# Kernel tuning notes

Measured on AMD Instinct MI355X. Metric: run time of the kernel, lower is better.

The kernel has to match this reference:

```python
import jax, jax.numpy as jnp
import numpy as np

B, NPG, DEG = 512, 128, 16          # graphs, nodes/graph, out-degree
N = B * NPG                          # 65536 nodes
E = N * DEG                          # 1048576 edges
IN_DIM, HID, HEADS = 11, 32, 4
K1 = int(np.ceil(0.8 * NPG))         # 103 nodes/graph after pool1
K2 = int(np.ceil(0.8 * K1))          # 83 nodes/graph after pool2


def gat_conv(x, src, dst, mask, W, a_s, a_d, b, n_nodes):
    # PyG GATConv (concat=True, add_self_loops=True, eval mode -> no dropout)
    xp = (x @ W).reshape(n_nodes, HEADS, HID)            # [N,H,C]
    as_ = jnp.einsum('nhc,hc->nh', xp, a_s)
    ad_ = jnp.einsum('nhc,hc->nh', xp, a_d)
    loop = jnp.arange(n_nodes)
    s = jnp.concatenate([src, loop])
    d = jnp.concatenate([dst, loop])
    m = jnp.concatenate([mask, jnp.ones(n_nodes, bool)])
    logit = jax.nn.leaky_relu(as_[s] + ad_[d], 0.2)      # [E+N,H]
    logit = jnp.where(m[:, None], logit, -1e9)
    mx = jax.ops.segment_max(logit, d, num_segments=n_nodes)
    ex = jnp.exp(logit - mx[d]) * m[:, None]
    den = jax.ops.segment_sum(ex, d, num_segments=n_nodes)
    alpha = ex / (den[d] + 1e-16)                        # segment softmax over dst
    out = jax.ops.segment_sum(alpha[:, :, None] * xp[s], d, num_segments=n_nodes)
    return out.reshape(n_nodes, HEADS * HID) + b


def topk_pool(x, src, dst, mask, w, npg, k):
    # PyG TopKPooling: score = tanh((x*w).sum(-1)/||w||); keep top ceil(ratio*n) per graph
    nb = x.shape[0] // npg
    score = jnp.tanh((x @ w) / jnp.linalg.norm(w))
    vals, idx = jax.lax.top_k(score.reshape(nb, npg), k)  # [B,k]
    perm = (idx + (jnp.arange(nb) * npg)[:, None]).reshape(-1)
    x_new = x[perm] * vals.reshape(-1, 1)
    remap = jnp.full(nb * npg, -1).at[perm].set(jnp.arange(nb * k))
    ns, nd = remap[src], remap[dst]
    m = mask & (ns >= 0) & (nd >= 0)
    return x_new, jnp.where(m, ns, 0), jnp.where(m, nd, 0), m


def setup_inputs():
    key = jax.random.key(0)
    ks = jax.random.split(key, 24)
    s = 0.05
    x = jax.random.normal(ks[0], (N, IN_DIM), jnp.float32)
    src = jnp.repeat(jnp.arange(N), DEG)
    dst = (src // NPG) * NPG + jax.random.randint(ks[1], (E,), 0, NPG)
    edge_index = jnp.stack([src, dst])
    edge_attr = jax.random.normal(ks[2], (E, 4), jnp.float32)
    batch = jnp.repeat(jnp.arange(B), NPG)
    p = dict(
        W_g1=jax.random.normal(ks[3], (IN_DIM, HEADS * HID), jnp.float32) * s,
        att_src1=jax.random.normal(ks[4], (HEADS, HID), jnp.float32) * s,
        att_dst1=jax.random.normal(ks[5], (HEADS, HID), jnp.float32) * s,
        b_g1=jnp.zeros((HEADS * HID,), jnp.float32),
        W_t1=jax.random.normal(ks[6], (HEADS * HID, HID), jnp.float32) * s,
        b_t1=jnp.zeros((HID,), jnp.float32),
        pool_w1=jax.random.normal(ks[7], (HID,), jnp.float32) * s,
        W_g2=jax.random.normal(ks[8], (HID, HEADS * HID), jnp.float32) * s,
        att_src2=jax.random.normal(ks[9], (HEADS, HID), jnp.float32) * s,
        att_dst2=jax.random.normal(ks[10], (HEADS, HID), jnp.float32) * s,
        b_g2=jnp.zeros((HEADS * HID,), jnp.float32),
        W_t2=jax.random.normal(ks[11], (HEADS * HID, HID), jnp.float32) * s,
        b_t2=jnp.zeros((HID,), jnp.float32),
        pool_w2=jax.random.normal(ks[12], (HID,), jnp.float32) * s,
        W_l1=jax.random.normal(ks[13], (2 * HID, 256), jnp.float32) * s,
        b_l1=jnp.zeros((256,), jnp.float32),
        W_l2=jax.random.normal(ks[14], (256, 1024), jnp.float32) * s,
        b_l2=jnp.zeros((1024,), jnp.float32),
        W_l3=jax.random.normal(ks[15], (1024, 1), jnp.float32) * s,
        b_l3=jnp.zeros((1,), jnp.float32),
    )
    return dict(x=x, edge_index=edge_index, edge_attr=edge_attr, batch=batch, **p)


def reference(x, edge_index, edge_attr, batch,
              W_g1, att_src1, att_dst1, b_g1, W_t1, b_t1, pool_w1,
              W_g2, att_src2, att_dst2, b_g2, W_t2, b_t2, pool_w2,
              W_l1, b_l1, W_l2, b_l2, W_l3, b_l3):
    # edge_attr is ignored (GATConv built without edge_dim); batch is implicit
    # in the fixed equal-size graph layout.  Eval mode -> dropout disabled.
    src, dst = edge_index[0], edge_index[1]
    mask = jnp.ones(E, bool)
    h = jax.nn.relu(gat_conv(x, src, dst, mask, W_g1, att_src1, att_dst1, b_g1, N))
    h = h @ W_t1 + b_t1
    h, src, dst, mask = topk_pool(h, src, dst, mask, pool_w1, NPG, K1)
    h1 = h.reshape(B, K1, HID)
    g1 = jnp.concatenate([h1.max(1), h1.mean(1)], axis=1)   # [B, 2*HID]
    h = jax.nn.relu(gat_conv(h, src, dst, mask, W_g2, att_src2, att_dst2, b_g2, B * K1))
    h = h @ W_t2 + b_t2
    h, src, dst, mask = topk_pool(h, src, dst, mask, pool_w2, K1, K2)
    h2 = h.reshape(B, K2, HID)
    g2 = jnp.concatenate([h2.max(1), h2.mean(1)], axis=1)
    g = g1 + g2
    g = jax.nn.relu(g @ W_l1 + b_l1)
    g = jax.nn.relu(g @ W_l2 + b_l2)
    return g @ W_l3 + b_l3                                   # [B,1]
```

## Files before the change

kernel.cpp:

```cpp
#include <hip/hip_runtime.h>
#include <math.h>

constexpr int NPGc  = 128;
constexpr int NG    = 512;
constexpr int EPGc  = 2048;
constexpr int ETOT  = 1048576;
constexpr int IND   = 11;
constexpr int HIDc  = 32;
constexpr int FD    = 128;
constexpr int K1c   = 103;
constexpr int K2c   = 83;
constexpr int NN    = NG * NPGc;
constexpr int N2c   = NG * K1c;
constexpr int EPAD  = 2432;
constexpr int SBCAP = 2560;
constexpr int OFFSTR= 264;

__device__ __forceinline__ float lrelu(float x){ return fmaxf(x, 0.2f*x); }

template<int KIN>
__device__ void foldDev(const float* __restrict__ Wg, const float* __restrict__ avs,
                        const float* __restrict__ avd, float* __restrict__ S, float* __restrict__ D, int t)
{
    if (t < KIN * 4) {
        int k = t >> 2, h = t & 3;
        float s = 0.f, d = 0.f;
        for (int j = 0; j < HIDc; j++) {
            float w = Wg[k*FD + h*HIDc + j];
            s = fmaf(w, avs[h*HIDc + j], s);
            d = fmaf(w, avd[h*HIDc + j], d);
        }
        S[t] = s; D[t] = d;
    }
}

__global__ __launch_bounds__(256) void k_prep(const int* __restrict__ ei,
    const float* __restrict__ W1g, const float* __restrict__ s1, const float* __restrict__ d1,
    const float* __restrict__ W2g, const float* __restrict__ s2, const float* __restrict__ d2,
    int* __restrict__ csrOff, unsigned char* __restrict__ csrSB,
    float* __restrict__ S1, float* __restrict__ D1, float* __restrict__ S2, float* __restrict__ D2)
{
    int b = blockIdx.x, t = threadIdx.x;
    if (b >= NG) {
        if (b == NG)     foldDev<IND>(W1g, s1, d1, S1, D1, t);
        else             foldDev<HIDc>(W2g, s2, d2, S2, D2, t);
        return;
    }
    int g = b;
    __shared__ int cnt[128], cur[128], offL[129];
    __shared__ __align__(16) unsigned char sbL[SBCAP];
    const int FILL1 = (int)0x80808080u;
    if (t < 128) cnt[t] = 0;
    if (t < SBCAP/16) ((int4*)sbL)[t] = make_int4(FILL1, FILL1, FILL1, FILL1);
    __syncthreads();
    const int* dstG = ei + ETOT + g * EPGc;
    int dnv[8];
    #pragma unroll
    for (int q = 0; q < 8; q++) {
        int e = t + 256*q;
        dnv[q] = dstG[e] - g * NPGc;
        atomicAdd(&cnt[dnv[q]], 1);
    }
    __syncthreads();
    if (t < 64) {
        int c0 = cnt[2*t], c1 = cnt[2*t + 1];
        int p0 = (c0 + 3) & ~3, p1 = (c1 + 3) & ~3;
        int ps = p0 + p1, P = ps;
        #pragma unroll
        for (int dl = 1; dl < 64; dl <<= 1) { int v = __shfl_up(P, dl); if (t >= dl) P += v; }
        int E0 = P - ps;
        offL[2*t] = E0; offL[2*t + 1] = E0 + p0;
        cur[2*t]  = E0; cur[2*t + 1]  = E0 + p0;
        if (t == 63) offL[128] = P;
    }
    __syncthreads();
    #pragma unroll
    for (int q = 0; q < 8; q++) {
        int e = t + 256*q;
        int pos = atomicAdd(&cur[dnv[q]], 1);
        sbL[pos] = (unsigned char)(e >> 4);
    }
    __syncthreads();
    if (t < SBCAP/16) ((int4*)(csrSB + (size_t)g * SBCAP))[t] = ((const int4*)sbL)[t];
    if (t <= 128) csrOff[g*OFFSTR + t] = offL[t];
    if (t < 128)  csrOff[g*OFFSTR + 132 + t] = cur[t];
}

template<int NNODE, int KIN>
__global__ __launch_bounds__(256) void k_gat(
    const float* __restrict__ xin, const float* __restrict__ Wg,
    const float* __restrict__ WsS, const float* __restrict__ WsD,
    const int* __restrict__ csrOff, const unsigned char* __restrict__ csrSB,
    const float* __restrict__ bias, const float* __restrict__ Wt,
    float* __restrict__ htp)
{
    int g = blockIdx.x, h = blockIdx.y, t = threadIdx.x;
    __shared__ __align__(16) float xpL[NNODE * 32];
    __shared__ __align__(16) float WL[KIN * 32];
    __shared__ __align__(16) unsigned char sbL[SBCAP];
    __shared__ float asL[NNODE + 1], adL[NNODE], mL[NNODE], dIL[NNODE];
    __shared__ unsigned short offL[NNODE + 1];

    const float* xg = xin + (size_t)g * NNODE * KIN;

    for (int i = t; i < KIN * 32; i += 256) { int k = i >> 5, c = i & 31; WL[i] = Wg[k*FD + h*32 + c]; }
    if (t <= NNODE) offL[t] = (unsigned short)csrOff[g*OFFSTR + t];
    if (t < SBCAP/16) ((int4*)sbL)[t] = ((const int4*)(csrSB + (size_t)g * SBCAP))[t];
    if (t == NNODE) asL[NNODE] = -1e30f;
    __syncthreads();

    for (int p = t; p < NNODE * 8; p += 256) {
        int n = p >> 3, c4 = p & 7;
        const float* xr = xg + (size_t)n * KIN;
        float4 acc = make_float4(0.f, 0.f, 0.f, 0.f);
        #pragma unroll
        for (int k = 0; k < KIN; k++) {
            float xv = xr[k];
            float4 w4 = *(const float4*)&WL[k*32 + c4*4];
            acc.x = fmaf(xv, w4.x, acc.x); acc.y = fmaf(xv, w4.y, acc.y);
            acc.z = fmaf(xv, w4.z, acc.z); acc.w = fmaf(xv, w4.w, acc.w);
        }
        ((float4*)xpL)[n*8 + (c4 ^ (n & 7))] = acc;
    }
    if (t < NNODE) {
        const float* xr = xg + (size_t)t * KIN;
        float s = 0.f, d = 0.f;
        #pragma unroll
        for (int k = 0; k < KIN; k++) { float v = xr[k]; s = fmaf(v, WsS[k*4 + h], s); d = fmaf(v, WsD[k*4 + h], d); }
        asL[t] = s; adL[t] = d;
    }
    __syncthreads();

    if (t < NNODE) {
        float as_n = asL[t], adn = adL[t];
        int lo = offL[t], hi = offL[t + 1];
        float mx = as_n;
        for (int i = lo; i < hi; i += 4) {
            unsigned int q4 = *(const unsigned int*)(sbL + i);
            float a0 = asL[q4 & 255], a1 = asL[(q4 >> 8) & 255];
            float a2 = asL[(q4 >> 16) & 255], a3 = asL[q4 >> 24];
            mx = fmaxf(fmaxf(fmaxf(fmaxf(mx, a0), a1), a2), a3);
        }
        float m = lrelu(mx + adn);
        float den = expf(lrelu(as_n + adn) - m);
        for (int i = lo; i < hi; i += 4) {
            unsigned int q4 = *(const unsigned int*)(sbL + i);
            den += expf(lrelu(asL[q4 & 255] + adn) - m);
            den += expf(lrelu(asL[(q4 >> 8) & 255] + adn) - m);
            den += expf(lrelu(asL[(q4 >> 16) & 255] + adn) - m);
            den += expf(lrelu(asL[q4 >> 24] + adn) - m);
        }
        mL[t] = m; dIL[t] = 1.f / (den + 1e-16f);
    }
    __syncthreads();

    const float4* X4 = (const float4*)xpL;
    float4 rv[4];
    #pragma unroll
    for (int r = 0; r < 4; r++) {
        int p = t + r*256;
        if (p < NNODE * 8) {
            int n = p >> 3, c4 = p & 7;
            float adn = adL[n], mn = mL[n];
            float w0 = expf(lrelu(asL[n] + adn) - mn);
            float4 v = X4[n*8 + (c4 ^ (n & 7))];
            float4 a; a.x = w0*v.x; a.y = w0*v.y; a.z = w0*v.z; a.w = w0*v.w;
            int lo = offL[n], hi = offL[n + 1];
            for (int s = lo; s < hi; s += 4) {
                unsigned int q4 = *(const unsigned int*)(sbL + s);
                int s0 = q4 & 255, s1 = (q4 >> 8) & 255, s2 = (q4 >> 16) & 255, s3 = q4 >> 24;
                float e0 = expf(lrelu(asL[s0] + adn) - mn);
                float e1 = expf(lrelu(asL[s1] + adn) - mn);
                float e2 = expf(lrelu(asL[s2] + adn) - mn);
                float e3 = expf(lrelu(asL[s3] + adn) - mn);
                int r0 = min(s0, NNODE-1), r1 = min(s1, NNODE-1);
                int r2 = min(s2, NNODE-1), r3 = min(s3, NNODE-1);
                float4 u0 = X4[r0*8 + (c4 ^ (r0 & 7))];
                a.x = fmaf(e0, u0.x, a.x); a.y = fmaf(e0, u0.y, a.y);
                a.z = fmaf(e0, u0.z, a.z); a.w = fmaf(e0, u0.w, a.w);
                float4 u1 = X4[r1*8 + (c4 ^ (r1 & 7))];
                a.x = fmaf(e1, u1.x, a.x); a.y = fmaf(e1, u1.y, a.y);
                a.z = fmaf(e1, u1.z, a.z); a.w = fmaf(e1, u1.w, a.w);
                float4 u2 = X4[r2*8 + (c4 ^ (r2 & 7))];
                a.x = fmaf(e2, u2.x, a.x); a.y = fmaf(e2, u2.y, a.y);
                a.z = fmaf(e2, u2.z, a.z); a.w = fmaf(e2, u2.w, a.w);
                float4 u3 = X4[r3*8 + (c4 ^ (r3 & 7))];
                a.x = fmaf(e3, u3.x, a.x); a.y = fmaf(e3, u3.y, a.y);
                a.z = fmaf(e3, u3.z, a.z); a.w = fmaf(e3, u3.w, a.w);
            }
            float inv = dIL[n];
            float4 bq = *(const float4*)(bias + h*32 + c4*4);
            rv[r].x = fmaxf(fmaf(a.x, inv, bq.x), 0.f);
            rv[r].y = fmaxf(fmaf(a.y, inv, bq.y), 0.f);
            rv[r].z = fmaxf(fmaf(a.z, inv, bq.z), 0.f);
            rv[r].w = fmaxf(fmaf(a.w, inv, bq.w), 0.f);
        }
    }
    __syncthreads();
    {
        float4* X4w = (float4*)xpL;
        #pragma unroll
        for (int r = 0; r < 4; r++) {
            int p = t + r*256;
            if (p < NNODE * 8) {
                int n = p >> 3, c4 = p & 7;
                X4w[n*8 + (c4 ^ (n & 7))] = rv[r];
            }
        }
    }
    __syncthreads();

    const int n0 = t >> 3, j4 = t & 7;
    const float* WtH = Wt + h*1024 + j4*4;
    float4 a0 = make_float4(0,0,0,0), a1 = a0, a2 = a0, a3 = a0;
    #pragma unroll
    for (int c4 = 0; c4 < 8; c4++) {
        const int sw = c4 ^ (n0 & 7);
        float4 x0 = X4[n0*8 + sw];
        float4 x1 = make_float4(0,0,0,0), x2v = x1, x3 = x1;
        if (n0 + 32 < NNODE) x1  = X4[(n0+32)*8 + sw];
        if (n0 + 64 < NNODE) x2v = X4[(n0+64)*8 + sw];
        if (n0 + 96 < NNODE) x3  = X4[(n0+96)*8 + sw];
        const float e0[4] = {x0.x, x0.y, x0.z, x0.w};
        const float e1[4] = {x1.x, x1.y, x1.z, x1.w};
        const float e2[4] = {x2v.x, x2v.y, x2v.z, x2v.w};
        const float e3[4] = {x3.x, x3.y, x3.z, x3.w};
        #pragma unroll
        for (int j = 0; j < 4; j++) {
            float4 w4 = *(const float4*)(WtH + (c4*4 + j)*32);
            a0.x = fmaf(e0[j], w4.x, a0.x); a0.y = fmaf(e0[j], w4.y, a0.y);
            a0.z = fmaf(e0[j], w4.z, a0.z); a0.w = fmaf(e0[j], w4.w, a0.w);
            a1.x = fmaf(e1[j], w4.x, a1.x); a1.y = fmaf(e1[j], w4.y, a1.y);
            a1.z = fmaf(e1[j], w4.z, a1.z); a1.w = fmaf(e1[j], w4.w, a1.w);
            a2.x = fmaf(e2[j], w4.x, a2.x); a2.y = fmaf(e2[j], w4.y, a2.y);
            a2.z = fmaf(e2[j], w4.z, a2.z); a2.w = fmaf(e2[j], w4.w, a2.w);
            a3.x = fmaf(e3[j], w4.x, a3.x); a3.y = fmaf(e3[j], w4.y, a3.y);
            a3.z = fmaf(e3[j], w4.z, a3.z); a3.w = fmaf(e3[j], w4.w, a3.w);
        }
    }
    {
        size_t base = ((size_t)(g * NNODE + n0) * 4 + h) * 32 + j4 * 4;
        *(float4*)(htp + base) = a0;
        if (n0 + 32 < NNODE) *(float4*)(htp + base + (size_t)32*128) = a1;
        if (n0 + 64 < NNODE) *(float4*)(htp + base + (size_t)64*128) = a2;
        if (n0 + 96 < NNODE) *(float4*)(htp + base + (size_t)96*128) = a3;
    }
}

template<int NIN, int KEEP, bool FIRST>
__global__ __launch_bounds__(256) void k_linpool(
    const float* __restrict__ htp, const float* __restrict__ bt, const float* __restrict__ pw,
    float* __restrict__ xnew, const int* __restrict__ ei,
    int* __restrict__ csrOffW, unsigned char* __restrict__ sbW,
    float* __restrict__ gfeat, const float* __restrict__ gprev,
    const float* __restrict__ W1, const float* __restrict__ b1,
    const float* __restrict__ W2, const float* __restrict__ b2,
    const float* __restrict__ W3, const float* __restrict__ b3,
    float* __restrict__ outp)
{
    int g = blockIdx.x, t = threadIdx.x;
    __shared__ float htL[NIN * 33];
    __shared__ float scoreL[NIN];
    __shared__ int rnkL[NIN];
    __shared__ int cnt[128], cur[128], offL[129];
    __shared__ __align__(16) unsigned char sbL[SBCAP];
    __shared__ float gvec[64];
    __shared__ float h1L[256], red[256];

    for (int p = t; p < NIN * 8; p += 256) {
        int n = p >> 3, q = p & 7;
        const float4* row = (const float4*)(htp + (size_t)(g * NIN + n) * 128);
        float4 s = ((const float4*)bt)[q];
        float4 p0 = row[q], p1 = row[8 + q], p2 = row[16 + q], p3 = row[24 + q];
        s.x += p0.x; s.y += p0.y; s.z += p0.z; s.w += p0.w;
        s.x += p1.x; s.y += p1.y; s.z += p1.z; s.w += p1.w;
        s.x += p2.x; s.y += p2.y; s.z += p2.z; s.w += p2.w;
        s.x += p3.x; s.y += p3.y; s.z += p3.z; s.w += p3.w;
        float* d = htL + n*33 + q*4;
        d[0] = s.x; d[1] = s.y; d[2] = s.z; d[3] = s.w;
    }
    __syncthreads();

    float nrm; { float ss = 0.f; for (int k = 0; k < HIDc; k++) { float w = pw[k]; ss = fmaf(w, w, ss); } nrm = sqrtf(ss); }
    if (t < NIN) {
        float dot = 0.f;
        for (int k = 0; k < HIDc; k++) dot = fmaf(htL[t*33 + k], pw[k], dot);
        scoreL[t] = tanhf(dot / nrm);
    }
    __syncthreads();
    if (t < NIN) {
        float si = scoreL[t]; int rank = 0;
        for (int q = 0; q < NIN; q++) {
            float sj = scoreL[q];
            rank += (sj > si || (sj == si && q < t)) ? 1 : 0;
        }
        rnkL[t] = (rank < KEEP) ? rank : -1;
    }
    __syncthreads();
    if constexpr (FIRST) {
        for (int p = t; p < NIN * 32; p += 256) {
            int n = p >> 5, jj = p & 31;
            int rk = rnkL[n];
            if (rk >= 0) xnew[((size_t)g*KEEP + rk)*HIDc + jj] = htL[n*33 + jj] * scoreL[n];
        }
    }
    if (t < HIDc) {
        float mx = -INFINITY, sm = 0.f;
        for (int n = 0; n < NIN; n++) {
            if (rnkL[n] >= 0) { float v = htL[n*33 + t] * scoreL[n]; mx = fmaxf(mx, v); sm += v; }
        }
        float mean = sm / (float)KEEP;
        if constexpr (FIRST) {
            gfeat[(size_t)g*64 + t]      = mx;
            gfeat[(size_t)g*64 + 32 + t] = mean;
        } else {
            gvec[t]      = gprev[(size_t)g*64 + t] + mx;
            gvec[32 + t] = gprev[(size_t)g*64 + 32 + t] + mean;
        }
    }

    if constexpr (FIRST) {
        __syncthreads();
        const int FILL2 = (int)0x67676767u;
        if (t < 128) cnt[t] = 0;
        if (t < SBCAP/16) ((int4*)sbL)[t] = make_int4(FILL2, FILL2, FILL2, FILL2);
        __syncthreads();
        const int* dstG = ei + ETOT + g * EPGc;
        int snv[8], dnv[8];
        #pragma unroll
        for (int q = 0; q < 8; q++) {
            int e = t + 256*q;
            int s = rnkL[e >> 4], d = rnkL[dstG[e] - g * NPGc];
            bool ok = (s >= 0 && d >= 0);
            snv[q] = s; dnv[q] = ok ? d : -1;
            if (ok) atomicAdd(&cnt[d], 1);
        }
        __syncthreads();
        if (t < 64) {
            int c0 = cnt[2*t], c1 = cnt[2*t + 1];
            int p0 = (c0 + 3) & ~3, p1 = (c1 + 3) & ~3;
            int ps = p0 + p1, P = ps;
            #pragma unroll
            for (int dl = 1; dl < 64; dl <<= 1) { int v = __shfl_up(P, dl); if (t >= dl) P += v; }
            int E0 = P - ps;
            offL[2*t] = E0; offL[2*t + 1] = E0 + p0;
            cur[2*t]  = E0; cur[2*t + 1]  = E0 + p0;
            if (t == 63) offL[128] = P;
        }
        __syncthreads();
        #pragma unroll
        for (int q = 0; q < 8; q++) {
            if (dnv[q] >= 0) {
                int pos = atomicAdd(&cur[dnv[q]], 1);
                sbL[pos] = (unsigned char)snv[q];
            }
        }
        __syncthreads();
        if (t < SBCAP/16) ((int4*)(sbW + (size_t)g * SBCAP))[t] = ((const int4*)sbL)[t];
        if (t <= K1c) csrOffW[g*OFFSTR + t] = offL[t];
        if (t < K1c)  csrOffW[g*OFFSTR + 132 + t] = cur[t];
    } else {
        __syncthreads();
        float a = b1[t];
        #pragma unroll 4
        for (int k = 0; k < 64; k++) a = fmaf(gvec[k], W1[k*256 + t], a);
        h1L[t] = fmaxf(a, 0.f);
        __syncthreads();
        float c0 = b2[t], c1 = b2[t + 256], c2 = b2[t + 512], c3 = b2[t + 768];
        const float* w2c = W2 + t;
        #pragma unroll 4
        for (int i = 0; i < 256; i++) {
            float hv = h1L[i];
            const float* wr = w2c + (size_t)i * 1024;
            c0 = fmaf(hv, wr[0],   c0);
            c1 = fmaf(hv, wr[256], c1);
            c2 = fmaf(hv, wr[512], c2);
            c3 = fmaf(hv, wr[768], c3);
        }
        float p = fmaf(fmaxf(c0, 0.f), W3[t],
                  fmaf(fmaxf(c1, 0.f), W3[t + 256],
                  fmaf(fmaxf(c2, 0.f), W3[t + 512],
                       fmaxf(c3, 0.f) * W3[t + 768])));
        red[t] = p;
        __syncthreads();
        for (int s = 128; s > 0; s >>= 1) { if (t < s) red[t] += red[t + s]; __syncthreads(); }
        if (t == 0) outp[g] = red[0] + b3[0];
    }
}

extern "C" void kernel_launch(void* const* d_in, const int* in_sizes, int n_in,
                              void* d_out, int out_size, void* d_ws, size_t ws_size,
                              hipStream_t stream)
{
    const float* x    = (const float*)d_in[0];
    const int*   ei   = (const int*)  d_in[1];
    const float* W_g1 = (const float*)d_in[4];
    const float* as1w = (const float*)d_in[5];
    const float* ad1w = (const float*)d_in[6];
    const float* b_g1 = (const float*)d_in[7];
    const float* W_t1 = (const float*)d_in[8];
    const float* b_t1 = (const float*)d_in[9];
    const float* pw1  = (const float*)d_in[10];
    const float* W_g2 = (const float*)d_in[11];
    const float* as2w = (const float*)d_in[12];
    const float* ad2w = (const float*)d_in[13];
    const float* b_g2 = (const float*)d_in[14];
    const float* W_t2 = (const float*)d_in[15];
    const float* b_t2 = (const float*)d_in[16];
    const float* pw2  = (const float*)d_in[17];
    const float* W_l1 = (const float*)d_in[18];
    const float* b_l1 = (const float*)d_in[19];
    const float* W_l2 = (const float*)d_in[20];
    const float* b_l2 = (const float*)d_in[21];
    const float* W_l3 = (const float*)d_in[22];
    const float* b_l3 = (const float*)d_in[23];
    float* out = (float*)d_out;

    char* ws = (char*)d_ws;
    size_t off = 0;
    auto alloc = [&](size_t bytes) -> void* {
        void* p = (void*)(ws + off);
        off += ((bytes + 255) / 256) * 256;
        return p;
    };
    float* htp1  = (float*)alloc((size_t)NN * 128 * 4);
    float* htp2  = (float*)alloc((size_t)N2c * 128 * 4);
    float* x2    = (float*)alloc((size_t)N2c * HIDc * 4);
    float* g1    = (float*)alloc((size_t)NG * 64 * 4);
    float* wsS1  = (float*)alloc(64 * 4);
    float* wsD1  = (float*)alloc(64 * 4);
    float* wsS2  = (float*)alloc(128 * 4);
    float* wsD2  = (float*)alloc(128 * 4);
    int*   off1  = (int*)  alloc((size_t)NG * OFFSTR * 4);
    unsigned char* sb1 = (unsigned char*)alloc((size_t)NG * SBCAP);
    int*   off2  = (int*)  alloc((size_t)NG * OFFSTR * 4);
    unsigned char* sb2 = (unsigned char*)alloc((size_t)NG * SBCAP);

    k_prep<<<NG + 2, 256, 0, stream>>>(ei, W_g1, as1w, ad1w, W_g2, as2w, ad2w,
                                       off1, sb1, wsS1, wsD1, wsS2, wsD2);

    k_gat<NPGc, IND><<<dim3(NG, 4), 256, 0, stream>>>(
        x, W_g1, wsS1, wsD1, off1, sb1, b_g1, W_t1, htp1);

    k_linpool<NPGc, K1c, true><<<NG, 256, 0, stream>>>(
        htp1, b_t1, pw1, x2, ei, off2, sb2, g1, nullptr,
        nullptr, nullptr, nullptr, nullptr, nullptr, nullptr, nullptr);

    k_gat<K1c, HIDc><<<dim3(NG, 4), 256, 0, stream>>>(
        x2, W_g2, wsS2, wsD2, off2, sb2, b_g2, W_t2, htp2);

    k_linpool<K1c, K2c, false><<<NG, 256, 0, stream>>>(
        htp2, b_t2, pw2, nullptr, nullptr, nullptr, nullptr, nullptr, g1,
        W_l1, b_l1, W_l2, b_l2, W_l3, b_l3, out);
}
```

Before: 322.8 us.

## Aggregate GAT messages with 2 threads per node over 16 channels each

The attention aggregation is remapped from 8 threads per node, each handling 4 channels, to 2 threads per node, each handling 16 channels. The per-edge exp and leaky-relu work is then computed 4x fewer times across the block, but each active thread does a longer serial loop and only 2*NNODE threads do work. The diff also adds a float4-vectorized input load when KIN is a multiple of 4 and restructures the Wt projection loop to do one node at a time with a single accumulator. Bank behaviour and occupancy may change with the new access pattern.

```diff
diff --git a/kernel.cpp b/kernel.cpp
--- a/kernel.cpp
+++ b/kernel.cpp
@@ -18,6 +18,20 @@
 
 __device__ __forceinline__ float lrelu(float x){ return fmaxf(x, 0.2f*x); }
 
+__device__ __forceinline__ void agg4(const float4* __restrict__ X4, int r, int cbase, float e,
+                                     float4& A0, float4& A1, float4& A2, float4& A3)
+{
+    int b = r * 8, s = r & 7;
+    float4 u0 = X4[b + ((cbase+0) ^ s)];
+    A0.x = fmaf(e, u0.x, A0.x); A0.y = fmaf(e, u0.y, A0.y); A0.z = fmaf(e, u0.z, A0.z); A0.w = fmaf(e, u0.w, A0.w);
+    float4 u1 = X4[b + ((cbase+1) ^ s)];
+    A1.x = fmaf(e, u1.x, A1.x); A1.y = fmaf(e, u1.y, A1.y); A1.z = fmaf(e, u1.z, A1.z); A1.w = fmaf(e, u1.w, A1.w);
+    float4 u2 = X4[b + ((cbase+2) ^ s)];
+    A2.x = fmaf(e, u2.x, A2.x); A2.y = fmaf(e, u2.y, A2.y); A2.z = fmaf(e, u2.z, A2.z); A2.w = fmaf(e, u2.w, A2.w);
+    float4 u3 = X4[b + ((cbase+3) ^ s)];
+    A3.x = fmaf(e, u3.x, A3.x); A3.y = fmaf(e, u3.y, A3.y); A3.z = fmaf(e, u3.z, A3.z); A3.w = fmaf(e, u3.w, A3.w);
+}
+
 template<int KIN>
 __device__ void foldDev(const float* __restrict__ Wg, const float* __restrict__ avs,
                         const float* __restrict__ avd, float* __restrict__ S, float* __restrict__ D, int t)
@@ -106,19 +120,36 @@
     for (int i = t; i < KIN * 32; i += 256) { int k = i >> 5, c = i & 31; WL[i] = Wg[k*FD + h*32 + c]; }
     if (t <= NNODE) offL[t] = (unsigned short)csrOff[g*OFFSTR + t];
     if (t < SBCAP/16) ((int4*)sbL)[t] = ((const int4*)(csrSB + (size_t)g * SBCAP))[t];
-    if (t == NNODE) asL[NNODE] = -1e30f;
+    if (t == 0) asL[NNODE] = -1e30f;
     __syncthreads();
 
     for (int p = t; p < NNODE * 8; p += 256) {
         int n = p >> 3, c4 = p & 7;
-        const float* xr = xg + (size_t)n * KIN;
         float4 acc = make_float4(0.f, 0.f, 0.f, 0.f);
-        #pragma unroll
-        for (int k = 0; k < KIN; k++) {
-            float xv = xr[k];
-            float4 w4 = *(const float4*)&WL[k*32 + c4*4];
-            acc.x = fmaf(xv, w4.x, acc.x); acc.y = fmaf(xv, w4.y, acc.y);
-            acc.z = fmaf(xv, w4.z, acc.z); acc.w = fmaf(xv, w4.w, acc.w);
+        if constexpr ((KIN & 3) == 0) {
+            const float4* xr4 = (const float4*)(xg + (size_t)n * KIN);
+            #pragma unroll
+            for (int k4 = 0; k4 < KIN/4; k4++) {
+                float4 xv = xr4[k4];
+                float4 w;
+                w = *(const float4*)&WL[(k4*4+0)*32 + c4*4];
+                acc.x = fmaf(xv.x, w.x, acc.x); acc.y = fmaf(xv.x, w.y, acc.y); acc.z = fmaf(xv.x, w.z, acc.z); acc.w = fmaf(xv.x, w.w, acc.w);
+                w = *(const float4*)&WL[(k4*4+1)*32 + c4*4];
+                acc.x = fmaf(xv.y, w.x, acc.x); acc.y = fmaf(xv.y, w.y, acc.y); acc.z = fmaf(xv.y, w.z, acc.z); acc.w = fmaf(xv.y, w.w, acc.w);
+                w = *(const float4*)&WL[(k4*4+2)*32 + c4*4];
+                acc.x = fmaf(xv.z, w.x, acc.x); acc.y = fmaf(xv.z, w.y, acc.y); acc.z = fmaf(xv.z, w.z, acc.z); acc.w = fmaf(xv.z, w.w, acc.w);
+                w = *(const float4*)&WL[(k4*4+3)*32 + c4*4];
+                acc.x = fmaf(xv.w, w.x, acc.x); acc.y = fmaf(xv.w, w.y, acc.y); acc.z = fmaf(xv.w, w.z, acc.z); acc.w = fmaf(xv.w, w.w, acc.w);
+            }
+        } else {
+            const float* xr = xg + (size_t)n * KIN;
+            #pragma unroll
+            for (int k = 0; k < KIN; k++) {
+                float xv = xr[k];
+                float4 w4 = *(const float4*)&WL[k*32 + c4*4];
+                acc.x = fmaf(xv, w4.x, acc.x); acc.y = fmaf(xv, w4.y, acc.y);
+                acc.z = fmaf(xv, w4.z, acc.z); acc.w = fmaf(xv, w4.w, acc.w);
+            }
         }
         ((float4*)xpL)[n*8 + (c4 ^ (n & 7))] = acc;
     }
@@ -155,95 +186,86 @@
     __syncthreads();
 
     const float4* X4 = (const float4*)xpL;
-    float4 rv[4];
-    #pragma unroll
-    for (int r = 0; r < 4; r++) {
-        int p = t + r*256;
-        if (p < NNODE * 8) {
-            int n = p >> 3, c4 = p & 7;
-            float adn = adL[n], mn = mL[n];
-            float w0 = expf(lrelu(asL[n] + adn) - mn);
-            float4 v = X4[n*8 + (c4 ^ (n & 7))];
-            float4 a; a.x = w0*v.x; a.y = w0*v.y; a.z = w0*v.z; a.w = w0*v.w;
-            int lo = offL[n], hi = offL[n + 1];
-            for (int s = lo; s < hi; s += 4) {
-                unsigned int q4 = *(const unsigned int*)(sbL + s);
-                int s0 = q4 & 255, s1 = (q4 >> 8) & 255, s2 = (q4 >> 16) & 255, s3 = q4 >> 24;
-                float e0 = expf(lrelu(asL[s0] + adn) - mn);
-                float e1 = expf(lrelu(asL[s1] + adn) - mn);
-                float e2 = expf(lrelu(asL[s2] + adn) - mn);
-                float e3 = expf(lrelu(asL[s3] + adn) - mn);
-                int r0 = min(s0, NNODE-1), r1 = min(s1, NNODE-1);
-                int r2 = min(s2, NNODE-1), r3 = min(s3, NNODE-1);
-                float4 u0 = X4[r0*8 + (c4 ^ (r0 & 7))];
-                a.x = fmaf(e0, u0.x, a.x); a.y = fmaf(e0, u0.y, a.y);
-                a.z = fmaf(e0, u0.z, a.z); a.w = fmaf(e0, u0.w, a.w);
-                float4 u1 = X4[r1*8 + (c4 ^ (r1 & 7))];
-                a.x = fmaf(e1, u1.x, a.x); a.y = fmaf(e1, u1.y, a.y);
-                a.z = fmaf(e1, u1.z, a.z); a.w = fmaf(e1, u1.w, a.w);
-                float4 u2 = X4[r2*8 + (c4 ^ (r2 & 7))];
-                a.x = fmaf(e2, u2.x, a.x); a.y = fmaf(e2, u2.y, a.y);
-                a.z = fmaf(e2, u2.z, a.z); a.w = fmaf(e2, u2.w, a.w);
-                float4 u3 = X4[r3*8 + (c4 ^ (r3 & 7))];
-                a.x = fmaf(e3, u3.x, a.x); a.y = fmaf(e3, u3.y, a.y);
-                a.z = fmaf(e3, u3.z, a.z); a.w = fmaf(e3, u3.w, a.w);
+    float4 A0, A1, A2, A3;
+    int n = 0, cbase = 0;
+    bool act = (t < NNODE * 2);
+    if (act) {
+        n = t >> 1; cbase = (t & 1) * 4;
+        float adn = adL[n], mn = mL[n];
+        float w0 = expf(lrelu(asL[n] + adn) - mn);
+        int sw = n & 7, nb = n * 8;
+        float4 v0 = X4[nb + ((cbase+0) ^ sw)];
+        A0 = make_float4(w0*v0.x, w0*v0.y, w0*v0.z, w0*v0.w);
+        float4 v1 = X4[nb + ((cbase+1) ^ sw)];
+        A1 = make_float4(w0*v1.x, w0*v1.y, w0*v1.z, w0*v1.w);
+        float4 v2 = X4[nb + ((cbase+2) ^ sw)];
+        A2 = make_float4(w0*v2.x, w0*v2.y, w0*v2.z, w0*v2.w);
+        float4 v3 = X4[nb + ((cbase+3) ^ sw)];
+        A3 = make_float4(w0*v3.x, w0*v3.y, w0*v3.z, w0*v3.w);
+        int lo = offL[n], hi = offL[n + 1];
+        for (int s = lo; s < hi; s += 4) {
+            unsigned int q4 = *(const unsigned int*)(sbL + s);
+            int s0 = q4 & 255, s1 = (q4 >> 8) & 255, s2 = (q4 >> 16) & 255, s3 = q4 >> 24;
+            float e0 = expf(lrelu(asL[s0] + adn) - mn);
+            float e1 = expf(lrelu(asL[s1] + adn) - mn);
+            float e2 = expf(lrelu(asL[s2] + adn) - mn);
+            float e3 = expf(lrelu(asL[s3] + adn) - mn);
+            agg4(X4, min(s0, NNODE-1), cbase, e0, A0, A1, A2, A3);
+            agg4(X4, min(s1, NNODE-1), cbase, e1, A0, A1, A2, A3);
+            agg4(X4, min(s2, NNODE-1), cbase, e2, A0, A1, A2, A3);
+            agg4(X4, min(s3, NNODE-1), cbase, e3, A0, A1, A2, A3);
+        }
+        float inv = dIL[n];
+        const float* bb = bias + h*32 + cbase*4;
+        float4 b0 = *(const float4*)(bb);
+        float4 b1 = *(const float4*)(bb + 4);
+        float4 b2 = *(const float4*)(bb + 8);
+        float4 b3 = *(const float4*)(bb + 12);
+        A0.x = fmaxf(fmaf(A0.x, inv, b0.x), 0.f); A0.y = fmaxf(fmaf(A0.y, inv, b0.y), 0.f);
+        A0.z = fmaxf(fmaf(A0.z, inv, b0.z), 0.f); A0.w = fmaxf(fmaf(A0.w, inv, b0.w), 0.f);
+        A1.x = fmaxf(fmaf(A1.x, inv, b1.x), 0.f); A1.y = fmaxf(fmaf(A1.y, inv, b1.y), 0.f);
+        A1.z = fmaxf(fmaf(A1.z, inv, b1.z), 0.f); A1.w = fmaxf(fmaf(A1.w, inv, b1.w), 0.f);
+        A2.x = fmaxf(fmaf(A2.x, inv, b2.x), 0.f); A2.y = fmaxf(fmaf(A2.y, inv, b2.y), 0.f);
+        A2.z = fmaxf(fmaf(A2.z, inv, b2.z), 0.f); A2.w = fmaxf(fmaf(A2.w, inv, b2.w), 0.f);
+        A3.x = fmaxf(fmaf(A3.x, inv, b3.x), 0.f); A3.y = fmaxf(fmaf(A3.y, inv, b3.y), 0.f);
+        A3.z = fmaxf(fmaf(A3.z, inv, b3.z), 0.f); A3.w = fmaxf(fmaf(A3.w, inv, b3.w), 0.f);
+    }
+    __syncthreads();
+    if (act) {
+        float4* X4w = (float4*)xpL;
+        int sw = n & 7, nb = n * 8;
+        X4w[nb + ((cbase+0) ^ sw)] = A0;
+        X4w[nb + ((cbase+1) ^ sw)] = A1;
+        X4w[nb + ((cbase+2) ^ sw)] = A2;
+        X4w[nb + ((cbase+3) ^ sw)] = A3;
+    }
+    __syncthreads();
+
+    {
+        const int n0 = t >> 3, j4 = t & 7;
+        const float* WtH = Wt + h*1024 + j4*4;
+        #pragma unroll
+        for (int rr = 0; rr < 4; rr++) {
+            int nn = n0 + rr*32;
+            if (nn < NNODE) {
+                float4 acc = make_float4(0.f, 0.f, 0.f, 0.f);
+                int sw = nn & 7, nb = nn * 8;
+                #pragma unroll
+                for (int c4 = 0; c4 < 8; c4++) {
+                    float4 xv = X4[nb + (c4 ^ sw)];
+                    float4 w;
+                    w = *(const float4*)(WtH + (c4*4+0)*32);
+                    acc.x = fmaf(xv.x, w.x, acc.x); acc.y = fmaf(xv.x, w.y, acc.y); acc.z = fmaf(xv.x, w.z, acc.z); acc.w = fmaf(xv.x, w.w, acc.w);
+                    w = *(const float4*)(WtH + (c4*4+1)*32);
+                    acc.x = fmaf(xv.y, w.x, acc.x); acc.y = fmaf(xv.y, w.y, acc.y); acc.z = fmaf(xv.y, w.z, acc.z); acc.w = fmaf(xv.y, w.w, acc.w);
+                    w = *(const float4*)(WtH + (c4*4+2)*32);
+                    acc.x = fmaf(xv.z, w.x, acc.x); acc.y = fmaf(xv.z, w.y, acc.y); acc.z = fmaf(xv.z, w.z, acc.z); acc.w = fmaf(xv.z, w.w, acc.w);
+                    w = *(const float4*)(WtH + (c4*4+3)*32);
+                    acc.x = fmaf(xv.w, w.x, acc.x); acc.y = fmaf(xv.w, w.y, acc.y); acc.z = fmaf(xv.w, w.z, acc.z); acc.w = fmaf(xv.w, w.w, acc.w);
+                }
+                *(float4*)(htp + ((size_t)(g * NNODE + nn) * 4 + h) * 32 + j4 * 4) = acc;
             }
-            float inv = dIL[n];
-            float4 bq = *(const float4*)(bias + h*32 + c4*4);
-            rv[r].x = fmaxf(fmaf(a.x, inv, bq.x), 0.f);
-            rv[r].y = fmaxf(fmaf(a.y, inv, bq.y), 0.f);
-            rv[r].z = fmaxf(fmaf(a.z, inv, bq.z), 0.f);
-            rv[r].w = fmaxf(fmaf(a.w, inv, bq.w), 0.f);
-        }
-    }
-    __syncthreads();
-    {
-        float4* X4w = (float4*)xpL;
-        #pragma unroll
-        for (int r = 0; r < 4; r++) {
-            int p = t + r*256;
-            if (p < NNODE * 8) {
-                int n = p >> 3, c4 = p & 7;
-                X4w[n*8 + (c4 ^ (n & 7))] = rv[r];
-            }
-        }
-    }
-    __syncthreads();
-
-    const int n0 = t >> 3, j4 = t & 7;
-    const float* WtH = Wt + h*1024 + j4*4;
-    float4 a0 = make_float4(0,0,0,0), a1 = a0, a2 = a0, a3 = a0;
-    #pragma unroll
-    for (int c4 = 0; c4 < 8; c4++) {
-        const int sw = c4 ^ (n0 & 7);
-        float4 x0 = X4[n0*8 + sw];
-        float4 x1 = make_float4(0,0,0,0), x2v = x1, x3 = x1;
-        if (n0 + 32 < NNODE) x1  = X4[(n0+32)*8 + sw];
-        if (n0 + 64 < NNODE) x2v = X4[(n0+64)*8 + sw];
-        if (n0 + 96 < NNODE) x3  = X4[(n0+96)*8 + sw];
-        const float e0[4] = {x0.x, x0.y, x0.z, x0.w};
-        const float e1[4] = {x1.x, x1.y, x1.z, x1.w};
-        const float e2[4] = {x2v.x, x2v.y, x2v.z, x2v.w};
-        const float e3[4] = {x3.x, x3.y, x3.z, x3.w};
-        #pragma unroll
-        for (int j = 0; j < 4; j++) {
-            float4 w4 = *(const float4*)(WtH + (c4*4 + j)*32);
-            a0.x = fmaf(e0[j], w4.x, a0.x); a0.y = fmaf(e0[j], w4.y, a0.y);
-            a0.z = fmaf(e0[j], w4.z, a0.z); a0.w = fmaf(e0[j], w4.w, a0.w);
-            a1.x = fmaf(e1[j], w4.x, a1.x); a1.y = fmaf(e1[j], w4.y, a1.y);
-            a1.z = fmaf(e1[j], w4.z, a1.z); a1.w = fmaf(e1[j], w4.w, a1.w);
-            a2.x = fmaf(e2[j], w4.x, a2.x); a2.y = fmaf(e2[j], w4.y, a2.y);
-            a2.z = fmaf(e2[j], w4.z, a2.z); a2.w = fmaf(e2[j], w4.w, a2.w);
-            a3.x = fmaf(e3[j], w4.x, a3.x); a3.y = fmaf(e3[j], w4.y, a3.y);
-            a3.z = fmaf(e3[j], w4.z, a3.z); a3.w = fmaf(e3[j], w4.w, a3.w);
-        }
-    }
-    {
-        size_t base = ((size_t)(g * NNODE + n0) * 4 + h) * 32 + j4 * 4;
-        *(float4*)(htp + base) = a0;
-        if (n0 + 32 < NNODE) *(float4*)(htp + base + (size_t)32*128) = a1;
-        if (n0 + 64 < NNODE) *(float4*)(htp + base + (size_t)64*128) = a2;
-        if (n0 + 96 < NNODE) *(float4*)(htp + base + (size_t)96*128) = a3;
+        }
     }
 }
 
```

Result: faster. 285.0 us (-11.7%).
